# Optimization experiments

Hardware: AMD Instinct MI355X
Metric: run time of the kernel (lower is better)

## Reference

```python
import jax, jax.numpy as jnp
import numpy as np

NUM_HEADS = 16
D_MODEL = 1024
D_K = D_MODEL // NUM_HEADS


def setup_inputs() -> dict:
    key = jax.random.key(0)
    ks = jax.random.split(key, 12)
    B, S = 2, 2048
    scale = 1.0 / np.sqrt(D_MODEL)
    inp = {
        "query": jax.random.normal(ks[0], (B, S, D_MODEL), jnp.float32),
        "key": jax.random.normal(ks[1], (B, S, D_MODEL), jnp.float32),
        "value": jax.random.normal(ks[2], (B, S, D_MODEL), jnp.float32),
        "mask": jnp.ones((B, S, S), jnp.int32),
        "Wq": jax.random.normal(ks[3], (D_MODEL, D_MODEL), jnp.float32) * scale,
        "bq": jax.random.normal(ks[4], (D_MODEL,), jnp.float32) * scale,
        "Wk": jax.random.normal(ks[5], (D_MODEL, D_MODEL), jnp.float32) * scale,
        "bk": jax.random.normal(ks[6], (D_MODEL,), jnp.float32) * scale,
        "Wv": jax.random.normal(ks[7], (D_MODEL, D_MODEL), jnp.float32) * scale,
        "bv": jax.random.normal(ks[8], (D_MODEL,), jnp.float32) * scale,
        "Wo": jax.random.normal(ks[9], (D_MODEL, D_MODEL), jnp.float32) * scale,
        "bo": jax.random.normal(ks[10], (D_MODEL,), jnp.float32) * scale,
    }
    return inp


def _split_heads(x):
    B, S, _ = x.shape
    return x.reshape(B, S, NUM_HEADS, D_K).transpose(0, 2, 1, 3)  # [B,H,S,d_k]


def reference(query, key, value, mask, Wq, bq, Wk, bk, Wv, bv, Wo, bo):
    # torch Linear: y = x @ W.T + b
    q = _split_heads(query @ Wq.T + bq)
    k = _split_heads(key @ Wk.T + bk)
    v = _split_heads(value @ Wv.T + bv)
    scores = jnp.einsum("bhqd,bhkd->bhqk", q, k) / np.sqrt(D_K)
    scores = jnp.where(mask[:, None, :, :] == 0, jnp.float32(-1e9), scores)
    p_attn = jax.nn.softmax(scores, axis=-1)
    attn = jnp.einsum("bhqk,bhkd->bhqd", p_attn, v)  # [B,H,S,d_k]
    B, _, S, _ = attn.shape
    x = attn.transpose(0, 2, 1, 3).reshape(B, S, D_MODEL)
    return x @ Wo.T + bo
```

## Files before the change

### kernel.cpp

```cpp
#include <hip/hip_runtime.h>
#include <hip/hip_bf16.h>
#include <cstdint>

#define DEVINL static __device__ __forceinline__

typedef __attribute__((ext_vector_type(4))) float floatx4;
typedef __attribute__((ext_vector_type(8))) short bf16x8;

DEVINL unsigned short f2bf(float f) {
    union { float f; uint32_t u; } v; v.f = f;
    return (unsigned short)((v.u + 0x7FFFu + ((v.u >> 16) & 1u)) >> 16);
}

DEVINL uint32_t pk2bf(float x, float y) {
    __hip_bfloat162 h = __float22bfloat162_rn(float2{x, y});
    union { __hip_bfloat162 h; uint32_t u; } v; v.h = h;
    return v.u;
}

DEVINL floatx4 mfma16(bf16x8 a, bf16x8 b, floatx4 c) {
    return __builtin_amdgcn_mfma_f32_16x16x32_bf16(a, b, c, 0, 0, 0);
}

#define GLDS16(g, l)                                                            \
    __builtin_amdgcn_global_load_lds(                                           \
        (const __attribute__((address_space(1))) void*)(g),                     \
        (__attribute__((address_space(3))) void*)(l), 16, 0, 0)

constexpr int B_ = 2, S_ = 2048, D_ = 1024, H_ = 16, DK_ = 64;
constexpr int BSROWS = B_ * S_;
constexpr int NQB = S_ / 128;
constexpr int NKT = S_ / 64;

__device__ int g_flags[B_ * NQB * NKT];

__global__ __launch_bounds__(256)
void mask_flags(const int* __restrict__ mask)
{
    int bid = blockIdx.x;
    int kt = bid & 31, qb = (bid >> 5) & 15, b = bid >> 9;
    const int* base = mask + (size_t)(b * S_ + qb * 128) * S_ + kt * 64;
    int ok = 1;
    #pragma unroll
    for (int i = 0; i < 8; ++i) {
        int u = threadIdx.x + 256 * i;
        int row = u >> 4, c = u & 15;
        int4 m = *(const int4*)(base + (size_t)row * S_ + c * 4);
        if ((m.x == 0) | (m.y == 0) | (m.z == 0) | (m.w == 0)) ok = 0;
    }
    __shared__ int f;
    if (threadIdx.x == 0) f = 1;
    __syncthreads();
    if (!ok) f = 0;
    __syncthreads();
    if (threadIdx.x == 0) g_flags[bid] = f;
}

__global__ __launch_bounds__(256)
void conv_wo(const float* __restrict__ W, unsigned short* __restrict__ Wb)
{
    int i = blockIdx.x * 256 + threadIdx.x;
    float4 v0 = *(const float4*)(W + (size_t)i * 8);
    float4 v1 = *(const float4*)(W + (size_t)i * 8 + 4);
    uint4 o;
    o.x = pk2bf(v0.x, v0.y); o.y = pk2bf(v0.z, v0.w);
    o.z = pk2bf(v1.x, v1.y); o.w = pk2bf(v1.z, v1.w);
    *(uint4*)(Wb + (size_t)i * 8) = o;
}

__global__ __launch_bounds__(256)
void gemm_qkv(const float* __restrict__ q, const float* __restrict__ k,
              const float* __restrict__ v,
              const float* __restrict__ Wq, const float* __restrict__ Wk,
              const float* __restrict__ Wv,
              const float* __restrict__ bq, const float* __restrict__ bk,
              const float* __restrict__ bv,
              unsigned short* __restrict__ Qp, unsigned short* __restrict__ KpF,
              unsigned short* __restrict__ VpF)
{
    constexpr int LD = 72;
    constexpr int K = D_, N = D_;
    __shared__ unsigned short As[128 * LD];
    __shared__ unsigned short Ws[64 * LD];

    const int z = blockIdx.z;
    const float* A    = z == 0 ? q  : z == 1 ? k  : v;
    const float* W    = z == 0 ? Wq : z == 1 ? Wk : Wv;
    const float* bias = z == 0 ? bq : z == 1 ? bk : bv;

    const int tid  = threadIdx.x;
    const int lane = tid & 63, wave = tid >> 6;
    const int lr = lane & 15, lg = lane >> 4;
    const int m0 = blockIdx.y * 128, n0 = blockIdx.x * 64;
    const int wm = (wave >> 1) * 64, wn = (wave & 1) * 32;

    floatx4 acc[4][2];
    #pragma unroll
    for (int mt = 0; mt < 4; ++mt)
        #pragma unroll
        for (int nt = 0; nt < 2; ++nt)
            acc[mt][nt] = floatx4{0.f, 0.f, 0.f, 0.f};

    float4 a4[8];
    float4 w4[4];

    auto load_tile = [&](int k0) {
        #pragma unroll
        for (int i = 0; i < 8; ++i) {
            int f = tid + 256 * i, row = f >> 4, c4 = f & 15;
            a4[i] = *(const float4*)(A + (size_t)(m0 + row) * K + k0 + c4 * 4);
        }
        #pragma unroll
        for (int i = 0; i < 4; ++i) {
            int f = tid + 256 * i, row = f >> 4, c4 = f & 15;
            w4[i] = *(const float4*)(W + (size_t)(n0 + row) * K + k0 + c4 * 4);
        }
    };
    auto store_tile = [&]() {
        #pragma unroll
        for (int i = 0; i < 8; ++i) {
            int f = tid + 256 * i, row = f >> 4, c4 = f & 15;
            uint2 p; p.x = pk2bf(a4[i].x, a4[i].y); p.y = pk2bf(a4[i].z, a4[i].w);
            *(uint2*)&As[row * LD + c4 * 4] = p;
        }
        #pragma unroll
        for (int i = 0; i < 4; ++i) {
            int f = tid + 256 * i, row = f >> 4, c4 = f & 15;
            uint2 p; p.x = pk2bf(w4[i].x, w4[i].y); p.y = pk2bf(w4[i].z, w4[i].w);
            *(uint2*)&Ws[row * LD + c4 * 4] = p;
        }
    };

    load_tile(0);
    for (int k0 = 0; k0 < K; k0 += 64) {
        store_tile();
        __syncthreads();
        if (k0 + 64 < K) load_tile(k0 + 64);

        #pragma unroll
        for (int kf = 0; kf < 2; ++kf) {
            bf16x8 af[4], bfr[2];
            #pragma unroll
            for (int mt = 0; mt < 4; ++mt)
                af[mt] = *(const bf16x8*)&As[(wm + mt * 16 + lr) * LD + kf * 32 + lg * 8];
            #pragma unroll
            for (int nt = 0; nt < 2; ++nt)
                bfr[nt] = *(const bf16x8*)&Ws[(wn + nt * 16 + lr) * LD + kf * 32 + lg * 8];
            #pragma unroll
            for (int mt = 0; mt < 4; ++mt)
                #pragma unroll
                for (int nt = 0; nt < 2; ++nt)
                    acc[mt][nt] = mfma16(af[mt], bfr[nt], acc[mt][nt]);
        }
        __syncthreads();
    }

    if (z == 0) {
        #pragma unroll
        for (int nt = 0; nt < 2; ++nt) {
            int col = n0 + wn + nt * 16 + lr;
            float bv2 = bias[col];
            #pragma unroll
            for (int mt = 0; mt < 4; ++mt)
                #pragma unroll
                for (int reg = 0; reg < 4; ++reg) {
                    int row = m0 + wm + mt * 16 + lg * 4 + reg;
                    Qp[(size_t)row * N + col] = f2bf((acc[mt][nt][reg] + bv2) * 0.125f);
                }
        }
    } else if (z == 1) {
        #pragma unroll
        for (int nt = 0; nt < 2; ++nt) {
            int c = n0 + wn + nt * 16 + lr;
            int h = c >> 6, d = c & 63;
            int kfA = d >> 5, lgA = (d >> 3) & 3, j = d & 7;
            float bv2 = bias[c];
            #pragma unroll
            for (int mt = 0; mt < 4; ++mt)
                #pragma unroll
                for (int reg = 0; reg < 4; ++reg) {
                    int t = m0 + wm + mt * 16 + lg * 4 + reg;
                    int bb = t >> 11, s = t & (S_ - 1);
                    int kt = s >> 6, key = s & 63;
                    int mtA = key >> 4, lrA = key & 15;
                    size_t off = (((size_t)(bb * 16 + h) * 32 + kt) * 8 + (kfA * 4 + mtA)) * 512
                               + (lrA + 16 * lgA) * 8 + j;
                    KpF[off] = f2bf(acc[mt][nt][reg] + bv2);
                }
        }
    } else {
        #pragma unroll
        for (int nt = 0; nt < 2; ++nt) {
            int c = n0 + wn + nt * 16 + lr;
            int h = c >> 6, dtA = (c >> 4) & 3;
            float bv2 = bias[c];
            #pragma unroll
            for (int mt = 0; mt < 4; ++mt) {
                int t0 = m0 + wm + mt * 16 + lg * 4;
                int bb = t0 >> 11, s0 = t0 & (S_ - 1);
                int kt = s0 >> 6, key = s0 & 63;
                int kfA = key >> 5, lgA = (key >> 3) & 3, j0 = key & 7;
                size_t off = (((size_t)(bb * 16 + h) * 32 + kt) * 8 + (dtA * 2 + kfA)) * 512
                           + (lr + 16 * lgA) * 8 + j0;
                uint2 p;
                p.x = pk2bf(acc[mt][nt][0] + bv2, acc[mt][nt][1] + bv2);
                p.y = pk2bf(acc[mt][nt][2] + bv2, acc[mt][nt][3] + bv2);
                *(uint2*)&VpF[off] = p;
            }
        }
    }
}

__global__ __launch_bounds__(256)
void attn_flash(const unsigned short* __restrict__ Qp,
                const unsigned short* __restrict__ KpF,
                const unsigned short* __restrict__ VpF,
                const int* __restrict__ mask,
                unsigned short* __restrict__ Out)
{
    constexpr int LD = 72;
    __shared__ unsigned short Ps[128 * LD];

    const int tid = threadIdx.x;
    const int lane = tid & 63, wave = tid >> 6;
    const int lr = lane & 15, lg = lane >> 4;
    const int h = blockIdx.x, qb = blockIdx.y, b = blockIdx.z;
    const int q0 = qb * 128, qw = q0 + wave * 32;

    bf16x8 qf[2][2];
    #pragma unroll
    for (int qt = 0; qt < 2; ++qt)
        #pragma unroll
        for (int kf = 0; kf < 2; ++kf)
            qf[qt][kf] = *(const bf16x8*)(Qp + (size_t)(b * S_ + qw + qt * 16 + lr) * D_ +
                                          h * DK_ + kf * 32 + lg * 8);

    float l_[2] = {0.f, 0.f};
    floatx4 o_acc[2][4];
    #pragma unroll
    for (int qt = 0; qt < 2; ++qt)
        #pragma unroll
        for (int dt = 0; dt < 4; ++dt) o_acc[qt][dt] = floatx4{0.f, 0.f, 0.f, 0.f};

    const unsigned short* kbase = KpF + (size_t)(b * 16 + h) * 32 * 4096 + lane * 8;
    const unsigned short* vbase = VpF + (size_t)(b * 16 + h) * 32 * 4096 + lane * 8;
    const int fbase = (b * NQB + qb) * NKT;
    unsigned short* PsW = &Ps[(wave * 32 + lr) * LD];

    for (int kt = 0; kt < NKT; ++kt) {
        const unsigned short* kb = kbase + kt * 4096;
        const unsigned short* vb = vbase + kt * 4096;
        bf16x8 kfr[8], vfr[8];
        #pragma unroll
        for (int c = 0; c < 8; ++c) kfr[c] = *(const bf16x8*)(kb + c * 512);
        #pragma unroll
        for (int c = 0; c < 8; ++c) vfr[c] = *(const bf16x8*)(vb + c * 512);

        floatx4 sc[2][4];
        #pragma unroll
        for (int qt = 0; qt < 2; ++qt)
            #pragma unroll
            for (int mt = 0; mt < 4; ++mt) sc[qt][mt] = floatx4{0.f, 0.f, 0.f, 0.f};
        #pragma unroll
        for (int mt = 0; mt < 4; ++mt)
            #pragma unroll
            for (int kf = 0; kf < 2; ++kf)
                #pragma unroll
                for (int qt = 0; qt < 2; ++qt)
                    sc[qt][mt] = mfma16(kfr[kf * 4 + mt], qf[qt][kf], sc[qt][mt]);

        if (g_flags[fbase + kt] == 0) {
            #pragma unroll
            for (int qt = 0; qt < 2; ++qt) {
                int qq = qw + qt * 16 + lr;
                const int* mrow = mask + (size_t)(b * S_ + qq) * S_ + kt * 64;
                #pragma unroll
                for (int mt = 0; mt < 4; ++mt)
                    #pragma unroll
                    for (int reg = 0; reg < 4; ++reg)
                        if (mrow[mt * 16 + lg * 4 + reg] == 0)
                            sc[qt][mt][reg] = -1e9f;
            }
        }

        #pragma unroll
        for (int qt = 0; qt < 2; ++qt) {
            #pragma unroll
            for (int mt = 0; mt < 4; ++mt) {
                float p0 = __expf(sc[qt][mt][0]), p1 = __expf(sc[qt][mt][1]);
                float p2 = __expf(sc[qt][mt][2]), p3 = __expf(sc[qt][mt][3]);
                l_[qt] += (p0 + p1) + (p2 + p3);
                uint2 pk; pk.x = pk2bf(p0, p1); pk.y = pk2bf(p2, p3);
                *(uint2*)&PsW[qt * 16 * LD + mt * 16 + lg * 4] = pk;
            }
        }

        bf16x8 pb[2][2];
        #pragma unroll
        for (int qt = 0; qt < 2; ++qt)
            #pragma unroll
            for (int kf = 0; kf < 2; ++kf)
                pb[qt][kf] = *(const bf16x8*)&PsW[qt * 16 * LD + kf * 32 + lg * 8];
        #pragma unroll
        for (int dt = 0; dt < 4; ++dt)
            #pragma unroll
            for (int kf = 0; kf < 2; ++kf)
                #pragma unroll
                for (int qt = 0; qt < 2; ++qt)
                    o_acc[qt][dt] = mfma16(vfr[dt * 2 + kf], pb[qt][kf], o_acc[qt][dt]);
    }

    #pragma unroll
    for (int qt = 0; qt < 2; ++qt) {
        float l = l_[qt];
        l += __shfl_xor(l, 16, 64);
        l += __shfl_xor(l, 32, 64);
        float inv = 1.f / l;
        int qq = qw + qt * 16 + lr;
        #pragma unroll
        for (int dt = 0; dt < 4; ++dt) {
            uint2 p;
            p.x = pk2bf(o_acc[qt][dt][0] * inv, o_acc[qt][dt][1] * inv);
            p.y = pk2bf(o_acc[qt][dt][2] * inv, o_acc[qt][dt][3] * inv);
            *(uint2*)&Out[(size_t)(b * S_ + qq) * D_ + h * DK_ + dt * 16 + lg * 4] = p;
        }
    }
}

__global__ __launch_bounds__(256)
void gemm_out(const unsigned short* __restrict__ Ap,
              const unsigned short* __restrict__ Wb,
              const float* __restrict__ bias, float* __restrict__ Cptr)
{
    constexpr int K = D_, N = D_;
    __shared__ unsigned short As[2][128 * 64];
    __shared__ unsigned short Wss[2][64 * 64];

    const int tid  = threadIdx.x;
    const int lane = tid & 63, wave = tid >> 6;
    const int lr = lane & 15, lg = lane >> 4;
    const int m0 = blockIdx.y * 128, n0 = blockIdx.x * 64;
    const int wm = (wave >> 1) * 64, wn = (wave & 1) * 32;

    int rowA[4], kcA[4], rowW[2], kcW[2];
    #pragma unroll
    for (int j = 0; j < 4; ++j) {
        int L = (wave * 4 + j) * 64 + lane;
        rowA[j] = L >> 3; kcA[j] = (L & 7) ^ (rowA[j] & 7);
    }
    #pragma unroll
    for (int j = 0; j < 2; ++j) {
        int L = (wave * 2 + j) * 64 + lane;
        rowW[j] = L >> 3; kcW[j] = (L & 7) ^ (rowW[j] & 7);
    }

    auto dma = [&](int k0, int buf) {
        #pragma unroll
        for (int j = 0; j < 4; ++j)
            GLDS16(Ap + (size_t)(m0 + rowA[j]) * K + k0 + kcA[j] * 8,
                   &As[buf][(wave * 4 + j) * 512 + lane * 8]);
        #pragma unroll
        for (int j = 0; j < 2; ++j)
            GLDS16(Wb + (size_t)(n0 + rowW[j]) * K + k0 + kcW[j] * 8,
                   &Wss[buf][(wave * 2 + j) * 512 + lane * 8]);
    };

    floatx4 acc[4][2];
    #pragma unroll
    for (int mt = 0; mt < 4; ++mt)
        #pragma unroll
        for (int nt = 0; nt < 2; ++nt)
            acc[mt][nt] = floatx4{0.f, 0.f, 0.f, 0.f};

    dma(0, 0);
    for (int it = 0; it < K / 64; ++it) {
        __syncthreads();
        if (it + 1 < K / 64) dma((it + 1) * 64, (it + 1) & 1);
        const int buf = it & 1;

        #pragma unroll
        for (int kf = 0; kf < 2; ++kf) {
            bf16x8 af[4], bfr[2];
            #pragma unroll
            for (int mt = 0; mt < 4; ++mt) {
                int row = wm + mt * 16 + lr;
                af[mt] = *(const bf16x8*)&As[buf][row * 64 + (((kf * 4 + lg) ^ (lr & 7)) * 8)];
            }
            #pragma unroll
            for (int nt = 0; nt < 2; ++nt) {
                int row = wn + nt * 16 + lr;
                bfr[nt] = *(const bf16x8*)&Wss[buf][row * 64 + (((kf * 4 + lg) ^ (lr & 7)) * 8)];
            }
            #pragma unroll
            for (int mt = 0; mt < 4; ++mt)
                #pragma unroll
                for (int nt = 0; nt < 2; ++nt)
                    acc[mt][nt] = mfma16(af[mt], bfr[nt], acc[mt][nt]);
        }
    }

    #pragma unroll
    for (int nt = 0; nt < 2; ++nt) {
        int col = n0 + wn + nt * 16 + lr;
        float bv2 = bias[col];
        #pragma unroll
        for (int mt = 0; mt < 4; ++mt)
            #pragma unroll
            for (int reg = 0; reg < 4; ++reg) {
                int row = m0 + wm + mt * 16 + lg * 4 + reg;
                Cptr[(size_t)row * N + col] = acc[mt][nt][reg] + bv2;
            }
    }
}

extern "C" void kernel_launch(void* const* d_in, const int* in_sizes, int n_in,
                              void* d_out, int out_size, void* d_ws, size_t ws_size,
                              hipStream_t stream)
{
    const float* query = (const float*)d_in[0];
    const float* key   = (const float*)d_in[1];
    const float* value = (const float*)d_in[2];
    const int*   mask  = (const int*)d_in[3];
    const float* Wq = (const float*)d_in[4];
    const float* bq = (const float*)d_in[5];
    const float* Wk = (const float*)d_in[6];
    const float* bk = (const float*)d_in[7];
    const float* Wv = (const float*)d_in[8];
    const float* bv = (const float*)d_in[9];
    const float* Wo = (const float*)d_in[10];
    const float* bo = (const float*)d_in[11];

    unsigned short* Qp  = (unsigned short*)d_ws;
    unsigned short* KpF = Qp  + (size_t)BSROWS * D_;
    unsigned short* VpF = KpF + (size_t)BSROWS * D_;
    unsigned short* Ap  = VpF + (size_t)BSROWS * D_;
    unsigned short* Wob = Ap  + (size_t)BSROWS * D_;

    dim3 blk(256);

    hipLaunchKernelGGL(mask_flags, dim3(B_ * NQB * NKT), blk, 0, stream, mask);
    hipLaunchKernelGGL(conv_wo, dim3(D_ * D_ / 8 / 256), blk, 0, stream, Wo, Wob);

    dim3 gqkv(D_ / 64, BSROWS / 128, 3);
    hipLaunchKernelGGL(gemm_qkv, gqkv, blk, 0, stream,
                       query, key, value, Wq, Wk, Wv, bq, bk, bv, Qp, KpF, VpF);

    dim3 gattn(H_, NQB, B_);
    hipLaunchKernelGGL(attn_flash, gattn, blk, 0, stream, Qp, KpF, VpF, mask, Ap);

    dim3 gout(D_ / 64, BSROWS / 128);
    hipLaunchKernelGGL(gemm_out, gout, blk, 0, stream, Ap, Wob, bo, (float*)d_out);
}
```

Measured before the change: 285.9 us.

## Pre-convert QKV inputs and weights to bf16, use async LDS DMA GEMM

A single prep kernel now converts query/key/value and all four weight matrices to bf16 and also computes the mask flags, replacing the separate mask and Wo conversion kernels. The QKV GEMM then loads bf16 tiles with global_load_lds into double-buffered, XOR-swizzled shared memory instead of loading fp32 through registers and converting inside the main loop. Both GEMMs remap block indices so that blocks sharing an XCD work on nearby M tiles, aiming for better L2 reuse. The trade-off is an extra full pass writing and re-reading bf16 copies of the activations, and the workspace is reused so the attention output overwrites the bf16 query buffer.

```diff
diff --git a/kernel.cpp b/kernel.cpp
--- a/kernel.cpp
+++ b/kernel.cpp
@@ -35,64 +35,105 @@
 __device__ int g_flags[B_ * NQB * NKT];
 
 __global__ __launch_bounds__(256)
-void mask_flags(const int* __restrict__ mask)
+void prep(const float* __restrict__ q, const float* __restrict__ k,
+          const float* __restrict__ v,
+          const float* __restrict__ Wq, const float* __restrict__ Wk,
+          const float* __restrict__ Wv, const float* __restrict__ Wo,
+          unsigned short* __restrict__ qb, unsigned short* __restrict__ kb,
+          unsigned short* __restrict__ vb,
+          unsigned short* __restrict__ wqb, unsigned short* __restrict__ wkb,
+          unsigned short* __restrict__ wvb, unsigned short* __restrict__ wob,
+          const int* __restrict__ mask)
 {
+    __shared__ int f;
     int bid = blockIdx.x;
-    int kt = bid & 31, qb = (bid >> 5) & 15, b = bid >> 9;
-    const int* base = mask + (size_t)(b * S_ + qb * 128) * S_ + kt * 64;
-    int ok = 1;
-    #pragma unroll
-    for (int i = 0; i < 8; ++i) {
-        int u = threadIdx.x + 256 * i;
-        int row = u >> 4, c = u & 15;
-        int4 m = *(const int4*)(base + (size_t)row * S_ + c * 4);
-        if ((m.x == 0) | (m.y == 0) | (m.z == 0) | (m.w == 0)) ok = 0;
-    }
-    __shared__ int f;
-    if (threadIdx.x == 0) f = 1;
-    __syncthreads();
-    if (!ok) f = 0;
-    __syncthreads();
-    if (threadIdx.x == 0) g_flags[bid] = f;
+    if (bid < 8192) {
+        const float* src; unsigned short* dst; int rb;
+        if      (bid < 2048) { src = q;  dst = qb;  rb = bid; }
+        else if (bid < 4096) { src = k;  dst = kb;  rb = bid - 2048; }
+        else if (bid < 6144) { src = v;  dst = vb;  rb = bid - 4096; }
+        else if (bid < 6656) { src = Wq; dst = wqb; rb = bid - 6144; }
+        else if (bid < 7168) { src = Wk; dst = wkb; rb = bid - 6656; }
+        else if (bid < 7680) { src = Wv; dst = wvb; rb = bid - 7168; }
+        else                 { src = Wo; dst = wob; rb = bid - 7680; }
+        size_t e = ((size_t)rb * 256 + threadIdx.x) * 8;
+        float4 v0 = *(const float4*)(src + e);
+        float4 v1 = *(const float4*)(src + e + 4);
+        uint4 o;
+        o.x = pk2bf(v0.x, v0.y); o.y = pk2bf(v0.z, v0.w);
+        o.z = pk2bf(v1.x, v1.y); o.w = pk2bf(v1.z, v1.w);
+        *(uint4*)(dst + e) = o;
+    } else {
+        int mb = bid - 8192;
+        int kt = mb & 31, qq = (mb >> 5) & 15, b = mb >> 9;
+        const int* base = mask + (size_t)(b * S_ + qq * 128) * S_ + kt * 64;
+        int ok = 1;
+        #pragma unroll
+        for (int i = 0; i < 8; ++i) {
+            int u = threadIdx.x + 256 * i;
+            int row = u >> 4, c = u & 15;
+            int4 m = *(const int4*)(base + (size_t)row * S_ + c * 4);
+            if ((m.x == 0) | (m.y == 0) | (m.z == 0) | (m.w == 0)) ok = 0;
+        }
+        if (threadIdx.x == 0) f = 1;
+        __syncthreads();
+        if (!ok) f = 0;
+        __syncthreads();
+        if (threadIdx.x == 0) g_flags[mb] = f;
+    }
 }
 
 __global__ __launch_bounds__(256)
-void conv_wo(const float* __restrict__ W, unsigned short* __restrict__ Wb)
-{
-    int i = blockIdx.x * 256 + threadIdx.x;
-    float4 v0 = *(const float4*)(W + (size_t)i * 8);
-    float4 v1 = *(const float4*)(W + (size_t)i * 8 + 4);
-    uint4 o;
-    o.x = pk2bf(v0.x, v0.y); o.y = pk2bf(v0.z, v0.w);
-    o.z = pk2bf(v1.x, v1.y); o.w = pk2bf(v1.z, v1.w);
-    *(uint4*)(Wb + (size_t)i * 8) = o;
-}
-
-__global__ __launch_bounds__(256)
-void gemm_qkv(const float* __restrict__ q, const float* __restrict__ k,
-              const float* __restrict__ v,
-              const float* __restrict__ Wq, const float* __restrict__ Wk,
-              const float* __restrict__ Wv,
+void gemm_qkv(const unsigned short* __restrict__ qb, const unsigned short* __restrict__ kb,
+              const unsigned short* __restrict__ vb,
+              const unsigned short* __restrict__ wqb, const unsigned short* __restrict__ wkb,
+              const unsigned short* __restrict__ wvb,
               const float* __restrict__ bq, const float* __restrict__ bk,
               const float* __restrict__ bv,
               unsigned short* __restrict__ Qp, unsigned short* __restrict__ KpF,
               unsigned short* __restrict__ VpF)
 {
-    constexpr int LD = 72;
     constexpr int K = D_, N = D_;
-    __shared__ unsigned short As[128 * LD];
-    __shared__ unsigned short Ws[64 * LD];
-
-    const int z = blockIdx.z;
-    const float* A    = z == 0 ? q  : z == 1 ? k  : v;
-    const float* W    = z == 0 ? Wq : z == 1 ? Wk : Wv;
-    const float* bias = z == 0 ? bq : z == 1 ? bk : bv;
+    __shared__ unsigned short As[2][128 * 64];
+    __shared__ unsigned short Wss[2][64 * 64];
+
+    const int bid = blockIdx.x;
+    const int xcd = bid & 7, sl = bid >> 3;
+    const int z = sl >> 6, rr = sl & 63;
+    const int nb = rr >> 2, mloc = rr & 3;
+    const int m0 = (mloc * 8 + xcd) * 128, n0 = nb * 64;
+
+    const unsigned short* A = z == 0 ? qb  : z == 1 ? kb  : vb;
+    const unsigned short* W = z == 0 ? wqb : z == 1 ? wkb : wvb;
+    const float* bias       = z == 0 ? bq  : z == 1 ? bk  : bv;
 
     const int tid  = threadIdx.x;
     const int lane = tid & 63, wave = tid >> 6;
     const int lr = lane & 15, lg = lane >> 4;
-    const int m0 = blockIdx.y * 128, n0 = blockIdx.x * 64;
     const int wm = (wave >> 1) * 64, wn = (wave & 1) * 32;
+
+    int rowA[4], kcA[4], rowW[2], kcW[2];
+    #pragma unroll
+    for (int j = 0; j < 4; ++j) {
+        int L = (wave * 4 + j) * 64 + lane;
+        rowA[j] = L >> 3; kcA[j] = (L & 7) ^ (rowA[j] & 7);
+    }
+    #pragma unroll
+    for (int j = 0; j < 2; ++j) {
+        int L = (wave * 2 + j) * 64 + lane;
+        rowW[j] = L >> 3; kcW[j] = (L & 7) ^ (rowW[j] & 7);
+    }
+
+    auto dma = [&](int k0, int buf) {
+        #pragma unroll
+        for (int j = 0; j < 4; ++j)
+            GLDS16(A + (size_t)(m0 + rowA[j]) * K + k0 + kcA[j] * 8,
+                   &As[buf][(wave * 4 + j) * 512 + lane * 8]);
+        #pragma unroll
+        for (int j = 0; j < 2; ++j)
+            GLDS16(W + (size_t)(n0 + rowW[j]) * K + k0 + kcW[j] * 8,
+                   &Wss[buf][(wave * 2 + j) * 512 + lane * 8]);
+    };
 
     floatx4 acc[4][2];
     #pragma unroll
@@ -101,58 +142,31 @@
         for (int nt = 0; nt < 2; ++nt)
             acc[mt][nt] = floatx4{0.f, 0.f, 0.f, 0.f};
 
-    float4 a4[8];
-    float4 w4[4];
-
-    auto load_tile = [&](int k0) {
-        #pragma unroll
-        for (int i = 0; i < 8; ++i) {
-            int f = tid + 256 * i, row = f >> 4, c4 = f & 15;
-            a4[i] = *(const float4*)(A + (size_t)(m0 + row) * K + k0 + c4 * 4);
-        }
-        #pragma unroll
-        for (int i = 0; i < 4; ++i) {
-            int f = tid + 256 * i, row = f >> 4, c4 = f & 15;
-            w4[i] = *(const float4*)(W + (size_t)(n0 + row) * K + k0 + c4 * 4);
-        }
-    };
-    auto store_tile = [&]() {
-        #pragma unroll
-        for (int i = 0; i < 8; ++i) {
-            int f = tid + 256 * i, row = f >> 4, c4 = f & 15;
-            uint2 p; p.x = pk2bf(a4[i].x, a4[i].y); p.y = pk2bf(a4[i].z, a4[i].w);
-            *(uint2*)&As[row * LD + c4 * 4] = p;
-        }
-        #pragma unroll
-        for (int i = 0; i < 4; ++i) {
-            int f = tid + 256 * i, row = f >> 4, c4 = f & 15;
-            uint2 p; p.x = pk2bf(w4[i].x, w4[i].y); p.y = pk2bf(w4[i].z, w4[i].w);
-            *(uint2*)&Ws[row * LD + c4 * 4] = p;
-        }
-    };
-
-    load_tile(0);
-    for (int k0 = 0; k0 < K; k0 += 64) {
-        store_tile();
+    dma(0, 0);
+    for (int it = 0; it < K / 64; ++it) {
         __syncthreads();
-        if (k0 + 64 < K) load_tile(k0 + 64);
+        if (it + 1 < K / 64) dma((it + 1) * 64, (it + 1) & 1);
+        const int buf = it & 1;
 
         #pragma unroll
         for (int kf = 0; kf < 2; ++kf) {
             bf16x8 af[4], bfr[2];
             #pragma unroll
-            for (int mt = 0; mt < 4; ++mt)
-                af[mt] = *(const bf16x8*)&As[(wm + mt * 16 + lr) * LD + kf * 32 + lg * 8];
-            #pragma unroll
-            for (int nt = 0; nt < 2; ++nt)
-                bfr[nt] = *(const bf16x8*)&Ws[(wn + nt * 16 + lr) * LD + kf * 32 + lg * 8];
+            for (int mt = 0; mt < 4; ++mt) {
+                int row = wm + mt * 16 + lr;
+                af[mt] = *(const bf16x8*)&As[buf][row * 64 + (((kf * 4 + lg) ^ (lr & 7)) * 8)];
+            }
+            #pragma unroll
+            for (int nt = 0; nt < 2; ++nt) {
+                int row = wn + nt * 16 + lr;
+                bfr[nt] = *(const bf16x8*)&Wss[buf][row * 64 + (((kf * 4 + lg) ^ (lr & 7)) * 8)];
+            }
             #pragma unroll
             for (int mt = 0; mt < 4; ++mt)
                 #pragma unroll
                 for (int nt = 0; nt < 2; ++nt)
                     acc[mt][nt] = mfma16(af[mt], bfr[nt], acc[mt][nt]);
         }
-        __syncthreads();
     }
 
     if (z == 0) {
@@ -180,8 +194,8 @@
                 #pragma unroll
                 for (int reg = 0; reg < 4; ++reg) {
                     int t = m0 + wm + mt * 16 + lg * 4 + reg;
-                    int bb = t >> 11, s = t & (S_ - 1);
-                    int kt = s >> 6, key = s & 63;
+                    int bb = t >> 11, sx = t & (S_ - 1);
+                    int kt = sx >> 6, key = sx & 63;
                     int mtA = key >> 4, lrA = key & 15;
                     size_t off = (((size_t)(bb * 16 + h) * 32 + kt) * 8 + (kfA * 4 + mtA)) * 512
                                + (lrA + 16 * lgA) * 8 + j;
@@ -336,10 +350,14 @@
     __shared__ unsigned short As[2][128 * 64];
     __shared__ unsigned short Wss[2][64 * 64];
 
+    const int bid = blockIdx.x;
+    const int xcd = bid & 7, sl = bid >> 3;
+    const int nb = sl >> 2, mloc = sl & 3;
+    const int m0 = (mloc * 8 + xcd) * 128, n0 = nb * 64;
+
     const int tid  = threadIdx.x;
     const int lane = tid & 63, wave = tid >> 6;
     const int lr = lane & 15, lg = lane >> 4;
-    const int m0 = blockIdx.y * 128, n0 = blockIdx.x * 64;
     const int wm = (wave >> 1) * 64, wn = (wave & 1) * 32;
 
     int rowA[4], kcA[4], rowW[2], kcW[2];
@@ -430,24 +448,29 @@
     const float* Wo = (const float*)d_in[10];
     const float* bo = (const float*)d_in[11];
 
-    unsigned short* Qp  = (unsigned short*)d_ws;
+    unsigned short* qb  = (unsigned short*)d_ws;
+    unsigned short* kb  = qb  + (size_t)BSROWS * D_;
+    unsigned short* vb  = kb  + (size_t)BSROWS * D_;
+    unsigned short* wqb = vb  + (size_t)BSROWS * D_;
+    unsigned short* wkb = wqb + (size_t)D_ * D_;
+    unsigned short* wvb = wkb + (size_t)D_ * D_;
+    unsigned short* wob = wvb + (size_t)D_ * D_;
+    unsigned short* Qp  = wob + (size_t)D_ * D_;
     unsigned short* KpF = Qp  + (size_t)BSROWS * D_;
     unsigned short* VpF = KpF + (size_t)BSROWS * D_;
-    unsigned short* Ap  = VpF + (size_t)BSROWS * D_;
-    unsigned short* Wob = Ap  + (size_t)BSROWS * D_;
+    unsigned short* Ap  = qb;
 
     dim3 blk(256);
 
-    hipLaunchKernelGGL(mask_flags, dim3(B_ * NQB * NKT), blk, 0, stream, mask);
-    hipLaunchKernelGGL(conv_wo, dim3(D_ * D_ / 8 / 256), blk, 0, stream, Wo, Wob);
-
-    dim3 gqkv(D_ / 64, BSROWS / 128, 3);
-    hipLaunchKernelGGL(gemm_qkv, gqkv, blk, 0, stream,
-                       query, key, value, Wq, Wk, Wv, bq, bk, bv, Qp, KpF, VpF);
+    hipLaunchKernelGGL(prep, dim3(8192 + 1024), blk, 0, stream,
+                       query, key, value, Wq, Wk, Wv, Wo,
+                       qb, kb, vb, wqb, wkb, wvb, wob, mask);
+
+    hipLaunchKernelGGL(gemm_qkv, dim3(1536), blk, 0, stream,
+                       qb, kb, vb, wqb, wkb, wvb, bq, bk, bv, Qp, KpF, VpF);
 
     dim3 gattn(H_, NQB, B_);
     hipLaunchKernelGGL(attn_flash, gattn, blk, 0, stream, Qp, KpF, VpF, mask, Ap);
 
-    dim3 gout(D_ / 64, BSROWS / 128);
-    hipLaunchKernelGGL(gemm_out, gout, blk, 0, stream, Ap, Wob, bo, (float*)d_out);
-}
+    hipLaunchKernelGGL(gemm_out, dim3(512), blk, 0, stream, Ap, wob, bo, (float*)d_out);
+}
```

Result: faster. 254.9 us (-10.9%).
